# Kernel optimization log

Hardware: AMD Instinct MI355X
Metric: run time of the kernel (lower is better)

Reference implementation:

```python
import jax, jax.numpy as jnp
import numpy as np

NUM_EMBEDDINGS = 1024
EMBEDDING_DIM = 64
COMMITMENT_COST = 0.25


def setup_inputs() -> dict:
    key = jax.random.key(0)
    kz, kc = jax.random.split(key)
    z = jax.random.normal(kz, (16, 2048, EMBEDDING_DIM), dtype=jnp.float32)
    # nn.Embedding weight init: uniform(-1/K, 1/K)
    codebook = (jax.random.uniform(kc, (NUM_EMBEDDINGS, EMBEDDING_DIM), dtype=jnp.float32) * 2.0 - 1.0) / NUM_EMBEDDINGS
    return {"z": z, "codebook": codebook}


def reference(z, codebook):
    D = codebook.shape[1]
    K = codebook.shape[0]
    flat_z = z.reshape(-1, D)  # [N, D]
    # squared L2 distances: ||z||^2 + ||e||^2 - 2 z.e  -> [N, K]
    distances = (
        jnp.sum(flat_z ** 2, axis=1, keepdims=True)
        + jnp.sum(codebook ** 2, axis=1)
        - 2.0 * jnp.matmul(flat_z, codebook.T)
    )
    encoding_indices = jnp.argmin(distances, axis=1)  # [N]
    quantized = codebook[encoding_indices].reshape(z.shape)

    e_latent_loss = jnp.mean((jax.lax.stop_gradient(quantized) - z) ** 2)
    q_latent_loss = jnp.mean((quantized - jax.lax.stop_gradient(z)) ** 2)
    vq_loss = q_latent_loss + COMMITMENT_COST * e_latent_loss

    # straight-through estimator
    quantized_st = z + jax.lax.stop_gradient(quantized - z)

    # perplexity from codebook usage histogram
    n = encoding_indices.shape[0]
    counts = jnp.zeros((K,), dtype=jnp.float32).at[encoding_indices].add(1.0)
    avg_probs = counts / n
    perplexity = jnp.exp(-jnp.sum(avg_probs * jnp.log(avg_probs + 1e-10)))

    indices_out = encoding_indices.reshape(z.shape[:-1])
    return quantized_st, vq_loss, indices_out, perplexity
```

## Files before the change

### kernel.cpp

```cpp
#include <hip/hip_runtime.h>
#include <math.h>


#define D 64
#define KC 1024
#define ROWS 64
#define TC 32
#define NT (KC / TC)
#define BCH 33

typedef short short8 __attribute__((ext_vector_type(8)));
typedef short short4v __attribute__((ext_vector_type(4)));
typedef float f32x4 __attribute__((ext_vector_type(4)));

__device__ __forceinline__ unsigned short f2bf(float x) {
  unsigned int u = __float_as_uint(x);
  unsigned int r = (u + 0x7fffu + ((u >> 16) & 1u)) >> 16;
  return (unsigned short)r;
}
__device__ __forceinline__ float bf2f(unsigned short h) {
  return __uint_as_float((unsigned int)h << 16);
}

__global__ __launch_bounds__(256) void vq_prep(
    const float* __restrict__ cb, unsigned short* __restrict__ bsplit,
    float* __restrict__ cbn, unsigned int* __restrict__ hist,
    float* __restrict__ loss_acc) {
  const int k = blockIdx.x * 256 + threadIdx.x;
  const float4* e = (const float4*)(cb + (size_t)k * D);
  unsigned short* bp = bsplit + (size_t)k * 128;
  float s0 = 0.f, s1 = 0.f, s2 = 0.f, s3 = 0.f;
#pragma unroll
  for (int i = 0; i < 16; ++i) {
    float4 v = e[i];
    s0 = fmaf(v.x, v.x, s0);
    s1 = fmaf(v.y, v.y, s1);
    s2 = fmaf(v.z, v.z, s2);
    s3 = fmaf(v.w, v.w, s3);
    unsigned short h0 = f2bf(v.x), h1 = f2bf(v.y), h2 = f2bf(v.z), h3 = f2bf(v.w);
    short4v hv = {(short)h0, (short)h1, (short)h2, (short)h3};
    short4v lv = {(short)f2bf(v.x - bf2f(h0)), (short)f2bf(v.y - bf2f(h1)),
                  (short)f2bf(v.z - bf2f(h2)), (short)f2bf(v.w - bf2f(h3))};
    *(short4v*)(bp + i * 4) = hv;
    *(short4v*)(bp + 64 + i * 4) = lv;
  }
  cbn[k] = (s0 + s1) + (s2 + s3);
  hist[k] = 0u;
  if (k == 0) loss_acc[0] = 0.f;
}

__global__ __launch_bounds__(256, 2) void vq_main(
    const float* __restrict__ z, const unsigned short* __restrict__ bsplit,
    const float* __restrict__ cbn, const float* __restrict__ cb,
    float* __restrict__ out_q, float* __restrict__ out_idx,
    unsigned int* __restrict__ hist, float* __restrict__ loss_acc) {
  __shared__ __align__(16) unsigned short Ash[ROWS * 136];
  __shared__ __align__(16) unsigned short Bsh[2][16 * BCH * 8];
  __shared__ float scbn[KC];
  __shared__ float srzp[ROWS * 16];
  __shared__ float srz[ROWS];
  __shared__ int skf[ROWS];
  __shared__ float swav[4];
  __shared__ unsigned int lhist[KC];

  const int tid = threadIdx.x;
  const int lane = tid & 63;
  const int wav = tid >> 6;
  const int quad = lane >> 4;
  const int col = lane & 15;
  const int rowbase = blockIdx.x * ROWS;

  const float4* z4 = (const float4*)(z + (size_t)rowbase * D);
#pragma unroll
  for (int it = 0; it < 4; ++it) {
    int f4 = it * 256 + tid;
    int row = f4 >> 4, c4 = (f4 & 15) * 4;
    float4 v = z4[f4];
    srzp[f4] = ((v.x * v.x + v.y * v.y) + (v.z * v.z + v.w * v.w));
    unsigned short h0 = f2bf(v.x), h1 = f2bf(v.y), h2 = f2bf(v.z), h3 = f2bf(v.w);
    short4v hv = {(short)h0, (short)h1, (short)h2, (short)h3};
    short4v lv = {(short)f2bf(v.x - bf2f(h0)), (short)f2bf(v.y - bf2f(h1)),
                  (short)f2bf(v.z - bf2f(h2)), (short)f2bf(v.w - bf2f(h3))};
    *(short4v*)&Ash[row * 136 + c4] = hv;
    *(short4v*)&Ash[row * 136 + 64 + c4] = lv;
  }
  *(float4*)&scbn[tid * 4] = *(const float4*)&cbn[tid * 4];
#pragma unroll
  for (int j = 0; j < KC / 256; ++j) lhist[tid + 256 * j] = 0u;

  const int cslot = (tid & 15) * BCH + (tid >> 4);
  {
    const size_t off = (size_t)(tid >> 4) * 128 + (size_t)(tid & 15) * 8;
    short8 s0 = *(const short8*)(bsplit + off);
    short8 s1 = *(const short8*)(bsplit + off + 2048);
    *(short8*)&Bsh[0][cslot * 8] = s0;
    *(short8*)&Bsh[0][(cslot + 16) * 8] = s1;
  }
  __syncthreads();
  if (tid < ROWS) {
    float s = 0.f;
#pragma unroll
    for (int i = 0; i < 16; ++i) s += srzp[tid * 16 + i];
    srz[tid] = s;
  }
  __syncthreads();

  const unsigned short* abase = &Ash[(wav * 16 + col) * 136 + quad * 8];
  const short8 a0 = *(const short8*)(abase + 0);
  const short8 a1 = *(const short8*)(abase + 32);
  const short8 a2 = *(const short8*)(abase + 64);
  const short8 a3 = *(const short8*)(abase + 96);

  float rzv[4];
#pragma unroll
  for (int reg = 0; reg < 4; ++reg) rzv[reg] = srz[wav * 16 + quad * 4 + reg];

  float b1d[4], b2d[4];
  int b1k[4], b2k[4];
#pragma unroll
  for (int i = 0; i < 4; ++i) {
    b1d[i] = 3.4e38f; b2d[i] = 3.4e38f;
    b1k[i] = 0x7fffffff; b2k[i] = 0x7fffffff;
  }

  for (int j = 0; j < NT; ++j) {
    const int kb = j * TC;
    const unsigned short* bcur = &Bsh[j & 1][0];
    short8 st0, st1;
    if (j + 1 < NT) {
      const size_t off = (size_t)((j + 1) * TC + (tid >> 4)) * 128 +
                         (size_t)(tid & 15) * 8;
      st0 = *(const short8*)(bsplit + off);
      st1 = *(const short8*)(bsplit + off + 2048);
    }
    const float enA = scbn[kb + col];
    const float enB = scbn[kb + 16 + col];
    const short8 bA0 = *(const short8*)(bcur + ((0 + quad) * BCH + col) * 8);
    const short8 bA1 = *(const short8*)(bcur + ((4 + quad) * BCH + col) * 8);
    const short8 bA2 = *(const short8*)(bcur + ((8 + quad) * BCH + col) * 8);
    const short8 bA3 = *(const short8*)(bcur + ((12 + quad) * BCH + col) * 8);
    const short8 bB0 = *(const short8*)(bcur + ((0 + quad) * BCH + col + 16) * 8);
    const short8 bB1 = *(const short8*)(bcur + ((4 + quad) * BCH + col + 16) * 8);
    const short8 bB2 = *(const short8*)(bcur + ((8 + quad) * BCH + col + 16) * 8);
    const short8 bB3 = *(const short8*)(bcur + ((12 + quad) * BCH + col + 16) * 8);

    f32x4 accA = {0.f, 0.f, 0.f, 0.f}, accB = {0.f, 0.f, 0.f, 0.f};
    accA = __builtin_amdgcn_mfma_f32_16x16x32_bf16(a0, bA0, accA, 0, 0, 0);
    accB = __builtin_amdgcn_mfma_f32_16x16x32_bf16(a0, bB0, accB, 0, 0, 0);
    accA = __builtin_amdgcn_mfma_f32_16x16x32_bf16(a1, bA1, accA, 0, 0, 0);
    accB = __builtin_amdgcn_mfma_f32_16x16x32_bf16(a1, bB1, accB, 0, 0, 0);
    accA = __builtin_amdgcn_mfma_f32_16x16x32_bf16(a2, bA0, accA, 0, 0, 0);
    accB = __builtin_amdgcn_mfma_f32_16x16x32_bf16(a2, bB0, accB, 0, 0, 0);
    accA = __builtin_amdgcn_mfma_f32_16x16x32_bf16(a3, bA1, accA, 0, 0, 0);
    accB = __builtin_amdgcn_mfma_f32_16x16x32_bf16(a3, bB1, accB, 0, 0, 0);
    accA = __builtin_amdgcn_mfma_f32_16x16x32_bf16(a0, bA2, accA, 0, 0, 0);
    accB = __builtin_amdgcn_mfma_f32_16x16x32_bf16(a0, bB2, accB, 0, 0, 0);
    accA = __builtin_amdgcn_mfma_f32_16x16x32_bf16(a1, bA3, accA, 0, 0, 0);
    accB = __builtin_amdgcn_mfma_f32_16x16x32_bf16(a1, bB3, accB, 0, 0, 0);

#pragma unroll
    for (int reg = 0; reg < 4; ++reg) {
      {
        float d = fmaf(-2.0f, accA[reg], rzv[reg] + enA);
        int k = kb + col;
        bool w1 = d < b1d[reg];
        bool w2 = d < b2d[reg];
        b2d[reg] = w1 ? b1d[reg] : (w2 ? d : b2d[reg]);
        b2k[reg] = w1 ? b1k[reg] : (w2 ? k : b2k[reg]);
        b1d[reg] = w1 ? d : b1d[reg];
        b1k[reg] = w1 ? k : b1k[reg];
      }
      {
        float d = fmaf(-2.0f, accB[reg], rzv[reg] + enB);
        int k = kb + 16 + col;
        bool w1 = d < b1d[reg];
        bool w2 = d < b2d[reg];
        b2d[reg] = w1 ? b1d[reg] : (w2 ? d : b2d[reg]);
        b2k[reg] = w1 ? b1k[reg] : (w2 ? k : b2k[reg]);
        b1d[reg] = w1 ? d : b1d[reg];
        b1k[reg] = w1 ? k : b1k[reg];
      }
    }

    if (j + 1 < NT) {
      unsigned short* bn = &Bsh[(j + 1) & 1][0];
      *(short8*)&bn[cslot * 8] = st0;
      *(short8*)&bn[(cslot + 16) * 8] = st1;
    }
    __syncthreads();
  }

#pragma unroll
  for (int m = 1; m < 16; m <<= 1) {
#pragma unroll
    for (int reg = 0; reg < 4; ++reg) {
      float od1 = __shfl_xor(b1d[reg], m, 64);
      int ok1 = __shfl_xor(b1k[reg], m, 64);
      float od2 = __shfl_xor(b2d[reg], m, 64);
      int ok2 = __shfl_xor(b2k[reg], m, 64);
      bool fo = (od1 < b1d[reg]) || (od1 == b1d[reg] && ok1 < b1k[reg]);
      float w1 = fo ? od1 : b1d[reg];
      int wk1 = fo ? ok1 : b1k[reg];
      float l1 = fo ? b1d[reg] : od1;
      int lk1 = fo ? b1k[reg] : ok1;
      bool so = (od2 < b2d[reg]) || (od2 == b2d[reg] && ok2 < b2k[reg]);
      float m2 = so ? od2 : b2d[reg];
      int mk2 = so ? ok2 : b2k[reg];
      bool lw = (l1 < m2) || (l1 == m2 && lk1 < mk2);
      b1d[reg] = w1;
      b1k[reg] = wk1;
      b2d[reg] = lw ? l1 : m2;
      b2k[reg] = lw ? lk1 : mk2;
    }
  }

  if (col < 4) {
    const int row = wav * 16 + quad * 4 + col;
    float bd1 = b1d[col], bd2 = b2d[col];
    int bk1 = b1k[col], bk2 = b2k[col];
    if (bd2 - bd1 < 1e-5f) {
      const int grow = rowbase + row;
      const float4* zp = (const float4*)(z + (size_t)grow * D);
      float s0 = 0.f, s1 = 0.f, s2 = 0.f, s3 = 0.f;
#pragma unroll
      for (int i = 0; i < 16; ++i) {
        float4 v = zp[i];
        s0 = fmaf(v.x, v.x, s0);
        s1 = fmaf(v.y, v.y, s1);
        s2 = fmaf(v.z, v.z, s2);
        s3 = fmaf(v.w, v.w, s3);
      }
      const float rzx = (s0 + s1) + (s2 + s3);
      float dx[2];
      int kk[2] = {bk1, bk2};
#pragma unroll
      for (int c = 0; c < 2; ++c) {
        const float4* e4 = (const float4*)(cb + (size_t)kk[c] * D);
        float d0 = 0.f, d1 = 0.f, d2 = 0.f, d3 = 0.f;
#pragma unroll
        for (int i = 0; i < 16; ++i) {
          float4 v = e4[i];
          float4 zv = zp[i];
          d0 = fmaf(zv.x, v.x, d0);
          d1 = fmaf(zv.y, v.y, d1);
          d2 = fmaf(zv.z, v.z, d2);
          d3 = fmaf(zv.w, v.w, d3);
        }
        float dot = (d0 + d1) + (d2 + d3);
        dx[c] = (rzx + scbn[kk[c]]) - 2.0f * dot;
      }
      if ((dx[1] < dx[0]) || (dx[1] == dx[0] && bk2 < bk1)) bk1 = bk2;
    }
    skf[row] = bk1;
    out_idx[rowbase + row] = (float)bk1;
    atomicAdd(&lhist[bk1], 1u);
  }
  __syncthreads();

#pragma unroll
  for (int j = 0; j < KC / 256; ++j) {
    unsigned int c = lhist[tid + 256 * j];
    if (c) atomicAdd(&hist[tid + 256 * j], c);
  }

  float lsum = 0.f;
#pragma unroll
  for (int it = 0; it < 4; ++it) {
    int f4 = it * 256 + tid;
    int r = f4 >> 4;
    int c4 = (f4 & 15) * 4;
    int bk = skf[r];
    const float4 q = *(const float4*)(cb + (size_t)bk * D + c4);
    const int grow = rowbase + r;
    const float4 zv = *(const float4*)(z + (size_t)grow * D + c4);
    *(float4*)(out_q + (size_t)grow * D + c4) = q;
    float ax = q.x - zv.x, ay = q.y - zv.y, az = q.z - zv.z, aw = q.w - zv.w;
    lsum += ax * ax + ay * ay + az * az + aw * aw;
  }
#pragma unroll
  for (int off = 32; off > 0; off >>= 1) lsum += __shfl_down(lsum, off, 64);
  if (lane == 0) swav[wav] = lsum;
  __syncthreads();
  if (tid == 0) {
    atomicAdd(loss_acc, (swav[0] + swav[1]) + (swav[2] + swav[3]));
  }
}

__global__ __launch_bounds__(1024) void vq_final(
    const unsigned int* __restrict__ hist, const float* __restrict__ loss_acc,
    float* __restrict__ out_loss, float* __restrict__ out_perp, float inv_n,
    float inv_nd) {
  __shared__ float part[16];
  const int t = threadIdx.x;
  const int lane = t & 63;
  const int wav = t >> 6;
  float p = (float)hist[t] * inv_n;
  float v = p * logf(p + 1e-10f);
#pragma unroll
  for (int off = 32; off > 0; off >>= 1) v += __shfl_down(v, off, 64);
  if (lane == 0) part[wav] = v;
  __syncthreads();
  if (t == 0) {
    float s = 0.f;
#pragma unroll
    for (int j = 0; j < 16; ++j) s += part[j];
    *out_perp = expf(-s);
    *out_loss = 1.25f * loss_acc[0] * inv_nd;
  }
}

extern "C" void kernel_launch(void* const* d_in, const int* in_sizes, int n_in,
                              void* d_out, int out_size, void* d_ws,
                              size_t ws_size, hipStream_t stream) {
  (void)n_in;
  (void)out_size;
  (void)ws_size;
  const float* z = (const float*)d_in[0];
  const float* cb = (const float*)d_in[1];
  const int N = in_sizes[0] / D;

  float* out_q = (float*)d_out;
  float* out_loss = (float*)d_out + (size_t)N * D;
  float* out_idx = out_loss + 1;
  float* out_perp = out_idx + N;

  unsigned int* hist = (unsigned int*)d_ws;
  float* loss_acc = (float*)d_ws + 1024;
  float* cbn = (float*)d_ws + 1040;
  unsigned short* bsplit = (unsigned short*)((float*)d_ws + 2064);

  vq_prep<<<dim3(KC / 256), dim3(256), 0, stream>>>(cb, bsplit, cbn, hist,
                                                    loss_acc);
  vq_main<<<dim3(N / ROWS), dim3(256), 0, stream>>>(z, bsplit, cbn, cb, out_q,
                                                    out_idx, hist, loss_acc);
  vq_final<<<dim3(1), dim3(1024), 0, stream>>>(
      hist, loss_acc, out_loss, out_perp, 1.0f / (float)N,
      1.0f / ((float)N * (float)D));
}
```

Baseline: 102.2 us.

## Split codebook scan across wave pairs, halve rows per block, fuse final reduction

Each block now handles 32 rows instead of 64. Pairs of waves split the codebook tiles, and their top-2 candidates are merged through shared memory. This doubles the grid to improve occupancy and latency hiding, and the MFMA chain is split into two accumulators to shorten dependencies. The separate final kernel is removed: the last block, found via an atomic done counter, computes perplexity and loss. The per-block shared histogram is replaced by direct global atomics, which may add contention. Fewer rows per block also mean the codebook tiles are streamed from global memory more times in total.

```diff
diff --git a/kernel.cpp b/kernel.cpp
--- a/kernel.cpp
+++ b/kernel.cpp
@@ -4,10 +4,11 @@
 
 #define D 64
 #define KC 1024
-#define ROWS 64
+#define ROWS 32
 #define TC 32
-#define NT (KC / TC)
+#define NP (KC / (2 * TC))
 #define BCH 33
+#define TILE_SH (16 * BCH * 8)
 
 typedef short short8 __attribute__((ext_vector_type(8)));
 typedef short short4v __attribute__((ext_vector_type(4)));
@@ -25,7 +26,7 @@
 __global__ __launch_bounds__(256) void vq_prep(
     const float* __restrict__ cb, unsigned short* __restrict__ bsplit,
     float* __restrict__ cbn, unsigned int* __restrict__ hist,
-    float* __restrict__ loss_acc) {
+    float* __restrict__ loss_acc, unsigned int* __restrict__ done) {
   const int k = blockIdx.x * 256 + threadIdx.x;
   const float4* e = (const float4*)(cb + (size_t)k * D);
   unsigned short* bp = bsplit + (size_t)k * 128;
@@ -46,33 +47,43 @@
   }
   cbn[k] = (s0 + s1) + (s2 + s3);
   hist[k] = 0u;
-  if (k == 0) loss_acc[0] = 0.f;
-}
-
-__global__ __launch_bounds__(256, 2) void vq_main(
+  if (k == 0) {
+    loss_acc[0] = 0.f;
+    done[0] = 0u;
+  }
+}
+
+__global__ __launch_bounds__(256, 3) void vq_main(
     const float* __restrict__ z, const unsigned short* __restrict__ bsplit,
     const float* __restrict__ cbn, const float* __restrict__ cb,
     float* __restrict__ out_q, float* __restrict__ out_idx,
-    unsigned int* __restrict__ hist, float* __restrict__ loss_acc) {
+    unsigned int* __restrict__ hist, float* __restrict__ loss_acc,
+    unsigned int* __restrict__ done, float* __restrict__ out_loss,
+    float* __restrict__ out_perp, float inv_n, float inv_nd) {
   __shared__ __align__(16) unsigned short Ash[ROWS * 136];
-  __shared__ __align__(16) unsigned short Bsh[2][16 * BCH * 8];
+  __shared__ __align__(16) unsigned short Bsh[2][2][TILE_SH];
   __shared__ float scbn[KC];
   __shared__ float srzp[ROWS * 16];
   __shared__ float srz[ROWS];
   __shared__ int skf[ROWS];
   __shared__ float swav[4];
-  __shared__ unsigned int lhist[KC];
+  __shared__ float md1[ROWS], md2[ROWS];
+  __shared__ int mkk1[ROWS], mkk2[ROWS];
+  __shared__ float fpart[4];
+  __shared__ int lastFlag;
 
   const int tid = threadIdx.x;
   const int lane = tid & 63;
   const int wav = tid >> 6;
+  const int g = wav >> 1;
+  const int h = wav & 1;
   const int quad = lane >> 4;
   const int col = lane & 15;
   const int rowbase = blockIdx.x * ROWS;
 
   const float4* z4 = (const float4*)(z + (size_t)rowbase * D);
 #pragma unroll
-  for (int it = 0; it < 4; ++it) {
+  for (int it = 0; it < 2; ++it) {
     int f4 = it * 256 + tid;
     int row = f4 >> 4, c4 = (f4 & 15) * 4;
     float4 v = z4[f4];
@@ -85,16 +96,16 @@
     *(short4v*)&Ash[row * 136 + 64 + c4] = lv;
   }
   *(float4*)&scbn[tid * 4] = *(const float4*)&cbn[tid * 4];
-#pragma unroll
-  for (int j = 0; j < KC / 256; ++j) lhist[tid + 256 * j] = 0u;
 
   const int cslot = (tid & 15) * BCH + (tid >> 4);
-  {
-    const size_t off = (size_t)(tid >> 4) * 128 + (size_t)(tid & 15) * 8;
+#pragma unroll
+  for (int T = 0; T < 2; ++T) {
+    const size_t off =
+        (size_t)(T * TC + (tid >> 4)) * 128 + (size_t)(tid & 15) * 8;
     short8 s0 = *(const short8*)(bsplit + off);
     short8 s1 = *(const short8*)(bsplit + off + 2048);
-    *(short8*)&Bsh[0][cslot * 8] = s0;
-    *(short8*)&Bsh[0][(cslot + 16) * 8] = s1;
+    *(short8*)&Bsh[0][T][cslot * 8] = s0;
+    *(short8*)&Bsh[0][T][(cslot + 16) * 8] = s1;
   }
   __syncthreads();
   if (tid < ROWS) {
@@ -105,7 +116,7 @@
   }
   __syncthreads();
 
-  const unsigned short* abase = &Ash[(wav * 16 + col) * 136 + quad * 8];
+  const unsigned short* abase = &Ash[(g * 16 + col) * 136 + quad * 8];
   const short8 a0 = *(const short8*)(abase + 0);
   const short8 a1 = *(const short8*)(abase + 32);
   const short8 a2 = *(const short8*)(abase + 64);
@@ -113,25 +124,30 @@
 
   float rzv[4];
 #pragma unroll
-  for (int reg = 0; reg < 4; ++reg) rzv[reg] = srz[wav * 16 + quad * 4 + reg];
+  for (int reg = 0; reg < 4; ++reg) rzv[reg] = srz[g * 16 + quad * 4 + reg];
 
   float b1d[4], b2d[4];
   int b1k[4], b2k[4];
 #pragma unroll
   for (int i = 0; i < 4; ++i) {
-    b1d[i] = 3.4e38f; b2d[i] = 3.4e38f;
-    b1k[i] = 0x7fffffff; b2k[i] = 0x7fffffff;
-  }
-
-  for (int j = 0; j < NT; ++j) {
-    const int kb = j * TC;
-    const unsigned short* bcur = &Bsh[j & 1][0];
-    short8 st0, st1;
-    if (j + 1 < NT) {
-      const size_t off = (size_t)((j + 1) * TC + (tid >> 4)) * 128 +
-                         (size_t)(tid & 15) * 8;
-      st0 = *(const short8*)(bsplit + off);
-      st1 = *(const short8*)(bsplit + off + 2048);
+    b1d[i] = 3.4e38f;
+    b2d[i] = 3.4e38f;
+    b1k[i] = 0x7fffffff;
+    b2k[i] = 0x7fffffff;
+  }
+
+  for (int p = 0; p < NP; ++p) {
+    const int kb = (p * 2 + h) * TC;
+    const unsigned short* bcur = &Bsh[p & 1][h][0];
+    short8 st00, st01, st10, st11;
+    if (p + 1 < NP) {
+      const size_t base = (size_t)((p + 1) * 2) * TC;
+      const size_t o0 = (base + (tid >> 4)) * 128 + (size_t)(tid & 15) * 8;
+      const size_t o1 = (base + TC + (tid >> 4)) * 128 + (size_t)(tid & 15) * 8;
+      st00 = *(const short8*)(bsplit + o0);
+      st01 = *(const short8*)(bsplit + o0 + 2048);
+      st10 = *(const short8*)(bsplit + o1);
+      st11 = *(const short8*)(bsplit + o1 + 2048);
     }
     const float enA = scbn[kb + col];
     const float enB = scbn[kb + 16 + col];
@@ -144,24 +160,25 @@
     const short8 bB2 = *(const short8*)(bcur + ((8 + quad) * BCH + col + 16) * 8);
     const short8 bB3 = *(const short8*)(bcur + ((12 + quad) * BCH + col + 16) * 8);
 
-    f32x4 accA = {0.f, 0.f, 0.f, 0.f}, accB = {0.f, 0.f, 0.f, 0.f};
-    accA = __builtin_amdgcn_mfma_f32_16x16x32_bf16(a0, bA0, accA, 0, 0, 0);
-    accB = __builtin_amdgcn_mfma_f32_16x16x32_bf16(a0, bB0, accB, 0, 0, 0);
-    accA = __builtin_amdgcn_mfma_f32_16x16x32_bf16(a1, bA1, accA, 0, 0, 0);
-    accB = __builtin_amdgcn_mfma_f32_16x16x32_bf16(a1, bB1, accB, 0, 0, 0);
-    accA = __builtin_amdgcn_mfma_f32_16x16x32_bf16(a2, bA0, accA, 0, 0, 0);
-    accB = __builtin_amdgcn_mfma_f32_16x16x32_bf16(a2, bB0, accB, 0, 0, 0);
-    accA = __builtin_amdgcn_mfma_f32_16x16x32_bf16(a3, bA1, accA, 0, 0, 0);
-    accB = __builtin_amdgcn_mfma_f32_16x16x32_bf16(a3, bB1, accB, 0, 0, 0);
-    accA = __builtin_amdgcn_mfma_f32_16x16x32_bf16(a0, bA2, accA, 0, 0, 0);
-    accB = __builtin_amdgcn_mfma_f32_16x16x32_bf16(a0, bB2, accB, 0, 0, 0);
-    accA = __builtin_amdgcn_mfma_f32_16x16x32_bf16(a1, bA3, accA, 0, 0, 0);
-    accB = __builtin_amdgcn_mfma_f32_16x16x32_bf16(a1, bB3, accB, 0, 0, 0);
+    f32x4 accA0 = {0.f, 0.f, 0.f, 0.f}, accA1 = {0.f, 0.f, 0.f, 0.f};
+    f32x4 accB0 = {0.f, 0.f, 0.f, 0.f}, accB1 = {0.f, 0.f, 0.f, 0.f};
+    accA0 = __builtin_amdgcn_mfma_f32_16x16x32_bf16(a0, bA0, accA0, 0, 0, 0);
+    accB0 = __builtin_amdgcn_mfma_f32_16x16x32_bf16(a0, bB0, accB0, 0, 0, 0);
+    accA1 = __builtin_amdgcn_mfma_f32_16x16x32_bf16(a1, bA1, accA1, 0, 0, 0);
+    accB1 = __builtin_amdgcn_mfma_f32_16x16x32_bf16(a1, bB1, accB1, 0, 0, 0);
+    accA0 = __builtin_amdgcn_mfma_f32_16x16x32_bf16(a2, bA0, accA0, 0, 0, 0);
+    accB0 = __builtin_amdgcn_mfma_f32_16x16x32_bf16(a2, bB0, accB0, 0, 0, 0);
+    accA1 = __builtin_amdgcn_mfma_f32_16x16x32_bf16(a3, bA1, accA1, 0, 0, 0);
+    accB1 = __builtin_amdgcn_mfma_f32_16x16x32_bf16(a3, bB1, accB1, 0, 0, 0);
+    accA0 = __builtin_amdgcn_mfma_f32_16x16x32_bf16(a0, bA2, accA0, 0, 0, 0);
+    accB0 = __builtin_amdgcn_mfma_f32_16x16x32_bf16(a0, bB2, accB0, 0, 0, 0);
+    accA1 = __builtin_amdgcn_mfma_f32_16x16x32_bf16(a1, bA3, accA1, 0, 0, 0);
+    accB1 = __builtin_amdgcn_mfma_f32_16x16x32_bf16(a1, bB3, accB1, 0, 0, 0);
 
 #pragma unroll
     for (int reg = 0; reg < 4; ++reg) {
       {
-        float d = fmaf(-2.0f, accA[reg], rzv[reg] + enA);
+        float d = fmaf(-2.0f, accA0[reg] + accA1[reg], rzv[reg] + enA);
         int k = kb + col;
         bool w1 = d < b1d[reg];
         bool w2 = d < b2d[reg];
@@ -171,7 +188,7 @@
         b1k[reg] = w1 ? k : b1k[reg];
       }
       {
-        float d = fmaf(-2.0f, accB[reg], rzv[reg] + enB);
+        float d = fmaf(-2.0f, accB0[reg] + accB1[reg], rzv[reg] + enB);
         int k = kb + 16 + col;
         bool w1 = d < b1d[reg];
         bool w2 = d < b2d[reg];
@@ -182,10 +199,13 @@
       }
     }
 
-    if (j + 1 < NT) {
-      unsigned short* bn = &Bsh[(j + 1) & 1][0];
-      *(short8*)&bn[cslot * 8] = st0;
-      *(short8*)&bn[(cslot + 16) * 8] = st1;
+    if (p + 1 < NP) {
+      unsigned short* bn0 = &Bsh[(p + 1) & 1][0][0];
+      unsigned short* bn1 = &Bsh[(p + 1) & 1][1][0];
+      *(short8*)&bn0[cslot * 8] = st00;
+      *(short8*)&bn0[(cslot + 16) * 8] = st01;
+      *(short8*)&bn1[cslot * 8] = st10;
+      *(short8*)&bn1[(cslot + 16) * 8] = st11;
     }
     __syncthreads();
   }
@@ -214,10 +234,38 @@
     }
   }
 
-  if (col < 4) {
-    const int row = wav * 16 + quad * 4 + col;
+  if (h == 1 && col < 4) {
+    const int row = g * 16 + quad * 4 + col;
+    md1[row] = b1d[col];
+    mkk1[row] = b1k[col];
+    md2[row] = b2d[col];
+    mkk2[row] = b2k[col];
+  }
+  __syncthreads();
+
+  if (h == 0 && col < 4) {
+    const int row = g * 16 + quad * 4 + col;
     float bd1 = b1d[col], bd2 = b2d[col];
     int bk1 = b1k[col], bk2 = b2k[col];
+    {
+      float od1 = md1[row];
+      int ok1 = mkk1[row];
+      float od2 = md2[row];
+      int ok2 = mkk2[row];
+      bool fo = (od1 < bd1) || (od1 == bd1 && ok1 < bk1);
+      float w1 = fo ? od1 : bd1;
+      int wk1 = fo ? ok1 : bk1;
+      float l1 = fo ? bd1 : od1;
+      int lk1 = fo ? bk1 : ok1;
+      bool so = (od2 < bd2) || (od2 == bd2 && ok2 < bk2);
+      float m2 = so ? od2 : bd2;
+      int mk2v = so ? ok2 : bk2;
+      bool lw = (l1 < m2) || (l1 == m2 && lk1 < mk2v);
+      bd1 = w1;
+      bk1 = wk1;
+      bd2 = lw ? l1 : m2;
+      bk2 = lw ? lk1 : mk2v;
+    }
     if (bd2 - bd1 < 1e-5f) {
       const int grow = rowbase + row;
       const float4* zp = (const float4*)(z + (size_t)grow * D);
@@ -253,19 +301,13 @@
     }
     skf[row] = bk1;
     out_idx[rowbase + row] = (float)bk1;
-    atomicAdd(&lhist[bk1], 1u);
-  }
-  __syncthreads();
-
-#pragma unroll
-  for (int j = 0; j < KC / 256; ++j) {
-    unsigned int c = lhist[tid + 256 * j];
-    if (c) atomicAdd(&hist[tid + 256 * j], c);
-  }
+    atomicAdd(&hist[bk1], 1u);
+  }
+  __syncthreads();
 
   float lsum = 0.f;
 #pragma unroll
-  for (int it = 0; it < 4; ++it) {
+  for (int it = 0; it < 2; ++it) {
     int f4 = it * 256 + tid;
     int r = f4 >> 4;
     int c4 = (f4 & 15) * 4;
@@ -283,29 +325,30 @@
   __syncthreads();
   if (tid == 0) {
     atomicAdd(loss_acc, (swav[0] + swav[1]) + (swav[2] + swav[3]));
-  }
-}
-
-__global__ __launch_bounds__(1024) void vq_final(
-    const unsigned int* __restrict__ hist, const float* __restrict__ loss_acc,
-    float* __restrict__ out_loss, float* __restrict__ out_perp, float inv_n,
-    float inv_nd) {
-  __shared__ float part[16];
-  const int t = threadIdx.x;
-  const int lane = t & 63;
-  const int wav = t >> 6;
-  float p = (float)hist[t] * inv_n;
-  float v = p * logf(p + 1e-10f);
-#pragma unroll
-  for (int off = 32; off > 0; off >>= 1) v += __shfl_down(v, off, 64);
-  if (lane == 0) part[wav] = v;
-  __syncthreads();
-  if (t == 0) {
-    float s = 0.f;
-#pragma unroll
-    for (int j = 0; j < 16; ++j) s += part[j];
-    *out_perp = expf(-s);
-    *out_loss = 1.25f * loss_acc[0] * inv_nd;
+    __threadfence();
+    unsigned int t = atomicAdd(done, 1u);
+    lastFlag = (t == gridDim.x - 1) ? 1 : 0;
+  }
+  __syncthreads();
+
+  if (lastFlag) {
+    __threadfence();
+    float v = 0.f;
+#pragma unroll
+    for (int j = 0; j < KC / 256; ++j) {
+      unsigned int c = atomicAdd(&hist[tid + 256 * j], 0u);
+      float pr = (float)c * inv_n;
+      v += pr * logf(pr + 1e-10f);
+    }
+#pragma unroll
+    for (int off = 32; off > 0; off >>= 1) v += __shfl_down(v, off, 64);
+    if (lane == 0) fpart[wav] = v;
+    __syncthreads();
+    if (tid == 0) {
+      float la = atomicAdd(loss_acc, 0.0f);
+      *out_perp = expf(-((fpart[0] + fpart[1]) + (fpart[2] + fpart[3])));
+      *out_loss = 1.25f * la * inv_nd;
+    }
   }
 }
 
@@ -326,14 +369,13 @@
 
   unsigned int* hist = (unsigned int*)d_ws;
   float* loss_acc = (float*)d_ws + 1024;
+  unsigned int* done = (unsigned int*)d_ws + 1025;
   float* cbn = (float*)d_ws + 1040;
   unsigned short* bsplit = (unsigned short*)((float*)d_ws + 2064);
 
   vq_prep<<<dim3(KC / 256), dim3(256), 0, stream>>>(cb, bsplit, cbn, hist,
-                                                    loss_acc);
-  vq_main<<<dim3(N / ROWS), dim3(256), 0, stream>>>(z, bsplit, cbn, cb, out_q,
-                                                    out_idx, hist, loss_acc);
-  vq_final<<<dim3(1), dim3(1024), 0, stream>>>(
-      hist, loss_acc, out_loss, out_perp, 1.0f / (float)N,
-      1.0f / ((float)N * (float)D));
-}
+                                                    loss_acc, done);
+  vq_main<<<dim3(N / ROWS), dim3(256), 0, stream>>>(
+      z, bsplit, cbn, cb, out_q, out_idx, hist, loss_acc, done, out_loss,
+      out_perp, 1.0f / (float)N, 1.0f / ((float)N * (float)D));
+}
```

New measurement: 219.8 us. +115.0%, slower.
